# Kernel tuning notes

Measured on AMD Instinct MI355X. Metric: run time of the kernel, lower is better.

The kernel has to match this reference:

```python
import jax, jax.numpy as jnp
import numpy as np

N_NODES = 50000
N_EDGES = 800000
N_FEAT = 128
HIDDEN = 64
N_LAYERS = 3
N_GRAPHS = 512
N_CLASSES = 10
BN_EPS = 1e-5


def setup_inputs() -> dict:
    key = jax.random.key(0)
    ks = jax.random.split(key, 16)
    s = 1.0 / np.sqrt(HIDDEN)
    inp = {
        "x": jax.random.normal(ks[0], (N_NODES, N_FEAT), dtype=jnp.float32),
        "edge_index": jax.random.randint(ks[1], (2, N_EDGES), 0, N_NODES, dtype=jnp.int32),
        "batch": jnp.sort(jax.random.randint(ks[2], (N_NODES,), 0, N_GRAPHS, dtype=jnp.int32)),
        "enc_w": jax.random.normal(ks[3], (N_FEAT, HIDDEN), dtype=jnp.float32) / np.sqrt(N_FEAT),
        "enc_b": jnp.zeros((HIDDEN,), dtype=jnp.float32),
        "eps": jnp.zeros((N_LAYERS,), dtype=jnp.float32),
        "conv_w1": jax.random.normal(ks[4], (N_LAYERS, HIDDEN, HIDDEN), dtype=jnp.float32) * s,
        "conv_b1": jnp.zeros((N_LAYERS, HIDDEN), dtype=jnp.float32),
        "conv_w2": jax.random.normal(ks[5], (N_LAYERS, HIDDEN, HIDDEN), dtype=jnp.float32) * s,
        "conv_b2": jnp.zeros((N_LAYERS, HIDDEN), dtype=jnp.float32),
        "bn_gamma": jnp.ones((N_LAYERS, HIDDEN), dtype=jnp.float32),
        "bn_beta": jnp.zeros((N_LAYERS, HIDDEN), dtype=jnp.float32),
        "lin_w": jax.random.normal(ks[6], (HIDDEN, N_CLASSES), dtype=jnp.float32) * s,
        "lin_b": jnp.zeros((N_CLASSES,), dtype=jnp.float32),
    }
    return inp


def reference(x, edge_index, batch, enc_w, enc_b, eps, conv_w1, conv_b1,
              conv_w2, conv_b2, bn_gamma, bn_beta, lin_w, lin_b):
    n = x.shape[0]
    src, dst = edge_index[0], edge_index[1]
    h = x @ enc_w + enc_b  # [N, H] encoder
    for l in range(N_LAYERS):
        # GINConv: sum-aggregate neighbor features, add (1+eps)*self, 2-layer MLP
        agg = jax.ops.segment_sum(h[src], dst, num_segments=n)
        z = (1.0 + eps[l]) * h + agg
        z = jnp.maximum(z @ conv_w1[l] + conv_b1[l], 0.0) @ conv_w2[l] + conv_b2[l]
        # BatchNorm1d (batch statistics) + ReLU; dropout omitted (eval mode)
        mean = jnp.mean(z, axis=0)
        var = jnp.mean(jnp.square(z - mean), axis=0)
        z = (z - mean) * jax.lax.rsqrt(var + BN_EPS) * bn_gamma[l] + bn_beta[l]
        h = jnp.maximum(z, 0.0)
    # global mean pool over graphs
    pooled = jax.ops.segment_sum(h, batch, num_segments=N_GRAPHS)
    counts = jax.ops.segment_sum(jnp.ones((n,), dtype=h.dtype), batch, num_segments=N_GRAPHS)
    pooled = pooled / jnp.maximum(counts, 1.0)[:, None]
    return pooled @ lin_w + lin_b  # [N_GRAPHS, N_CLASSES]
```

## Files before the change

kernel.cpp:

```cpp
#include <hip/hip_runtime.h>

#define N_NODES   50000
#define N_EDGES   800000
#define N_FEAT    128
#define HIDDEN    64
#define N_LAYERS  3
#define N_GRAPHS  512
#define N_CLASSES 10
#define BN_EPS    1e-5f
#define SCAN_BLK  196
#define LWAVES    8
#define HP        32
#define NBLK      1024
#define QSCALE    65536.0f
#define QINV      (1.0f / 65536.0f)

__device__ __forceinline__ int swz(int c, int g) { return g ^ (c & 15); }

__device__ __forceinline__ unsigned bf16rne(float x)
{
    unsigned u = __float_as_uint(x);
    return (u + 0x7fffu + ((u >> 16) & 1u)) >> 16;
}
__device__ __forceinline__ float2 bf2(unsigned u)
{
    float2 r;
    r.x = __uint_as_float(u << 16);
    r.y = __uint_as_float(u & 0xffff0000u);
    return r;
}

__global__ __launch_bounds__(512, 6) void enc_kernel(
    const float* __restrict__ x, const float* __restrict__ w,
    const float* __restrict__ b, unsigned* __restrict__ h,
    int* __restrict__ deg)
{
    __shared__ __align__(16) float wT[HIDDEN * N_FEAT];
    __shared__ __align__(16) float xb[LWAVES][4][N_FEAT];
    {
        int g = blockIdx.x * 512 + threadIdx.x;
        if (g < N_NODES) deg[g] = 0;
    }
    for (int i = threadIdx.x; i < N_FEAT * HIDDEN; i += 512) {
        int k = i >> 6, c = i & 63;
        wT[c * 128 + swz(c, k >> 2) * 4 + (k & 3)] = w[i];
    }
    const int lane = threadIdx.x & 63;
    const int wv   = threadIdx.x >> 6;
    const int sz   = lane & 15;
    const int r2   = lane >> 5;
    const int cc   = (lane & 31) * 4;
    const float bias = b[lane];
    __syncthreads();
    const int nwaves = gridDim.x * LWAVES;
    for (int grp = blockIdx.x * LWAVES + wv; grp < N_NODES / 4; grp += nwaves) {
        const int nbase = grp * 4;
        float4 v0 = *(const float4*)&x[(size_t)(nbase + r2) * N_FEAT + cc];
        float4 v1 = *(const float4*)&x[(size_t)(nbase + 2 + r2) * N_FEAT + cc];
        *((float4*)&xb[wv][r2][cc])     = v0;
        *((float4*)&xb[wv][2 + r2][cc]) = v1;
        float o0 = bias, o1 = bias, o2 = bias, o3 = bias;
        #pragma unroll 8
        for (int kc = 0; kc < N_FEAT / 4; ++kc) {
            float4 w4 = *(const float4*)&wT[lane * 128 + ((kc ^ sz) << 2)];
            float4 z0 = *(const float4*)&xb[wv][0][4 * kc];
            float4 z1 = *(const float4*)&xb[wv][1][4 * kc];
            float4 z2 = *(const float4*)&xb[wv][2][4 * kc];
            float4 z3 = *(const float4*)&xb[wv][3][4 * kc];
            o0 = fmaf(w4.x, z0.x, fmaf(w4.y, z0.y, fmaf(w4.z, z0.z, fmaf(w4.w, z0.w, o0))));
            o1 = fmaf(w4.x, z1.x, fmaf(w4.y, z1.y, fmaf(w4.z, z1.z, fmaf(w4.w, z1.w, o1))));
            o2 = fmaf(w4.x, z2.x, fmaf(w4.y, z2.y, fmaf(w4.z, z2.z, fmaf(w4.w, z2.w, o2))));
            o3 = fmaf(w4.x, z3.x, fmaf(w4.y, z3.y, fmaf(w4.z, z3.z, fmaf(w4.w, z3.w, o3))));
        }
        float t0 = __shfl_xor(o0, 1), t1 = __shfl_xor(o1, 1);
        float t2 = __shfl_xor(o2, 1), t3 = __shfl_xor(o3, 1);
        if (!(lane & 1)) {
            int p = lane >> 1;
            h[(size_t)(nbase + 0) * HP + p] = bf16rne(o0) | (bf16rne(t0) << 16);
            h[(size_t)(nbase + 1) * HP + p] = bf16rne(o1) | (bf16rne(t1) << 16);
            h[(size_t)(nbase + 2) * HP + p] = bf16rne(o2) | (bf16rne(t2) << 16);
            h[(size_t)(nbase + 3) * HP + p] = bf16rne(o3) | (bf16rne(t3) << 16);
        }
    }
}

__global__ __launch_bounds__(256) void hist_kernel(const int* __restrict__ ei,
                                                   int* __restrict__ deg)
{
    int e = blockIdx.x * 256 + threadIdx.x;
    if (e < N_EDGES) atomicAdd(&deg[ei[N_EDGES + e]], 1);
}

__global__ __launch_bounds__(256) void scan1_kernel(const int* __restrict__ deg,
                                                    int* __restrict__ row_start,
                                                    int* __restrict__ bsum)
{
    __shared__ int s[256];
    const int tid = threadIdx.x;
    const int gid = blockIdx.x * 256 + tid;
    int v = (gid < N_NODES) ? deg[gid] : 0;
    s[tid] = v;
    __syncthreads();
    for (int off = 1; off < 256; off <<= 1) {
        int t = (tid >= off) ? s[tid - off] : 0;
        __syncthreads();
        if (tid >= off) s[tid] += t;
        __syncthreads();
    }
    if (gid < N_NODES) row_start[gid] = s[tid] - v;
    if (tid == 255) bsum[blockIdx.x] = s[255];
}

__global__ __launch_bounds__(256) void scan2_kernel(int* __restrict__ bsum,
                                                    int* __restrict__ row_start)
{
    __shared__ int s[256];
    const int tid = threadIdx.x;
    int v = (tid < SCAN_BLK) ? bsum[tid] : 0;
    s[tid] = v;
    __syncthreads();
    for (int off = 1; off < 256; off <<= 1) {
        int t = (tid >= off) ? s[tid - off] : 0;
        __syncthreads();
        if (tid >= off) s[tid] += t;
        __syncthreads();
    }
    if (tid < SCAN_BLK) bsum[tid] = s[tid] - v;
    if (tid == 255) row_start[N_NODES] = s[255];
}

__global__ __launch_bounds__(256) void scan3_kernel(int* __restrict__ row_start,
                                                    const int* __restrict__ bsum,
                                                    int* __restrict__ cursor)
{
    int gid = blockIdx.x * 256 + threadIdx.x;
    if (gid < N_NODES) {
        int v = row_start[gid] + bsum[blockIdx.x];
        row_start[gid] = v;
        cursor[gid] = v;
    }
}

__global__ __launch_bounds__(256) void fill_kernel(const int* __restrict__ ei,
                                                   int* __restrict__ cursor,
                                                   int* __restrict__ csr_src)
{
    int e = blockIdx.x * 256 + threadIdx.x;
    if (e >= N_EDGES) return;
    int d = ei[N_EDGES + e];
    int pos = atomicAdd(&cursor[d], 1);
    csr_src[pos] = ei[e];
}

template<bool HASBN>
__global__ __launch_bounds__(512, 8) void layer_kernel(
    const unsigned* __restrict__ hin, const int* __restrict__ csr_src,
    const int* __restrict__ row_start,
    const float* __restrict__ stats_prev, const float* __restrict__ gamma,
    const float* __restrict__ beta,
    const float* __restrict__ eps, int layer,
    const float* __restrict__ w1, const float* __restrict__ b1,
    const float* __restrict__ w2, const float* __restrict__ b2,
    unsigned* __restrict__ hout, float* __restrict__ partials)
{
    __shared__ __align__(16) float wT1[HIDDEN * HIDDEN];
    __shared__ __align__(16) float wT2[HIDDEN * HIDDEN];
    __shared__ __align__(16) float zb[LWAVES][4][HIDDEN];
    for (int i = threadIdx.x; i < HIDDEN * HIDDEN; i += 512) {
        int k = i >> 6, c = i & 63;
        int dst = c * 64 + swz(c, k >> 2) * 4 + (k & 3);
        wT1[dst] = w1[i];
        wT2[dst] = w2[i];
    }
    const int lane = threadIdx.x & 63;
    const int wv   = threadIdx.x >> 6;
    const int o    = lane >> 3;
    const int c8   = (lane & 7) * 4;
    const int cb   = c8 * 2;
    const int sz   = lane & 15;
    float Ag[8], Bg[8];
    #pragma unroll
    for (int t = 0; t < 8; ++t) { Ag[t] = 1.f; Bg[t] = 0.f; }
    if (HASBN) {
        const float invN = 1.0f / (float)N_NODES;
        #pragma unroll
        for (int t = 0; t < 8; ++t) {
            float mean = stats_prev[cb + t] * invN;
            float var  = stats_prev[HIDDEN + cb + t] * invN - mean * mean;
            float inv  = rsqrtf(fmaxf(var, 0.f) + BN_EPS);
            Ag[t] = inv * gamma[cb + t];
            Bg[t] = beta[cb + t] - mean * Ag[t];
        }
    }
    const float sf  = 1.0f + eps[layer];
    const float b1c = b1[lane], b2c = b2[lane];
    __syncthreads();

    float s = 0.f, s2 = 0.f;
    const int nwaves = gridDim.x * LWAVES;
    for (int grp = blockIdx.x * LWAVES + wv; grp < N_NODES / 4; grp += nwaves) {
        const int nbase = grp * 4;
        #pragma unroll
        for (int n = 0; n < 4; ++n) {
            const int node = nbase + n;
            const int s0 = row_start[node];
            const int s1 = row_start[node + 1];
            int a[8];
            #pragma unroll
            for (int t = 0; t < 8; ++t) a[t] = 0;
            for (int jb = s0; jb < s1; jb += 64) {
                int m = s1 - jb; if (m > 64) m = 64;
                int idx = csr_src[jb + (lane < m ? lane : m - 1)];
                int mm = m & ~7;
                for (int j = 0; j < mm; j += 8) {
                    int i = __shfl(idx, j + o);
                    uint4 u = *(const uint4*)&hin[(size_t)i * HP + c8];
                    float2 f0 = bf2(u.x), f1 = bf2(u.y), f2 = bf2(u.z), f3 = bf2(u.w);
                    float v[8] = {f0.x, f0.y, f1.x, f1.y, f2.x, f2.y, f3.x, f3.y};
                    #pragma unroll
                    for (int t = 0; t < 8; ++t) {
                        float f = v[t];
                        if (HASBN) f = fmaxf(fmaf(f, Ag[t], Bg[t]), 0.f);
                        a[t] += (int)(f * QSCALE);
                    }
                }
                int r8 = m & 7;
                if (r8) {
                    int sl = mm + o;
                    int i = __shfl(idx, sl < m ? sl : m - 1);
                    if (o < r8) {
                        uint4 u = *(const uint4*)&hin[(size_t)i * HP + c8];
                        float2 f0 = bf2(u.x), f1 = bf2(u.y), f2 = bf2(u.z), f3 = bf2(u.w);
                        float v[8] = {f0.x, f0.y, f1.x, f1.y, f2.x, f2.y, f3.x, f3.y};
                        #pragma unroll
                        for (int t = 0; t < 8; ++t) {
                            float f = v[t];
                            if (HASBN) f = fmaxf(fmaf(f, Ag[t], Bg[t]), 0.f);
                            a[t] += (int)(f * QSCALE);
                        }
                    }
                }
            }
            #pragma unroll
            for (int t = 0; t < 8; ++t) {
                a[t] += __shfl_xor(a[t], 8);
                a[t] += __shfl_xor(a[t], 16);
                a[t] += __shfl_xor(a[t], 32);
            }
            if (o == 0) {
                uint4 su = *(const uint4*)&hin[(size_t)node * HP + c8];
                float2 g0 = bf2(su.x), g1 = bf2(su.y), g2 = bf2(su.z), g3 = bf2(su.w);
                float svv[8] = {g0.x, g0.y, g1.x, g1.y, g2.x, g2.y, g3.x, g3.y};
                float zo[8];
                #pragma unroll
                for (int t = 0; t < 8; ++t) {
                    float f = svv[t];
                    if (HASBN) f = fmaxf(fmaf(f, Ag[t], Bg[t]), 0.f);
                    zo[t] = fmaf(sf, f, (float)a[t] * QINV);
                }
                float4 q0 = {zo[0], zo[1], zo[2], zo[3]};
                float4 q1 = {zo[4], zo[5], zo[6], zo[7]};
                *((float4*)&zb[wv][n][cb])     = q0;
                *((float4*)&zb[wv][n][cb + 4]) = q1;
            }
        }
        float o0 = b1c, o1 = b1c, o2 = b1c, o3 = b1c;
        #pragma unroll 4
        for (int kc = 0; kc < HIDDEN / 4; ++kc) {
            float4 w4 = *(const float4*)&wT1[lane * 64 + ((kc ^ sz) << 2)];
            float4 z0 = *(const float4*)&zb[wv][0][4 * kc];
            float4 z1 = *(const float4*)&zb[wv][1][4 * kc];
            float4 z2 = *(const float4*)&zb[wv][2][4 * kc];
            float4 z3 = *(const float4*)&zb[wv][3][4 * kc];
            o0 = fmaf(w4.x, z0.x, fmaf(w4.y, z0.y, fmaf(w4.z, z0.z, fmaf(w4.w, z0.w, o0))));
            o1 = fmaf(w4.x, z1.x, fmaf(w4.y, z1.y, fmaf(w4.z, z1.z, fmaf(w4.w, z1.w, o1))));
            o2 = fmaf(w4.x, z2.x, fmaf(w4.y, z2.y, fmaf(w4.z, z2.z, fmaf(w4.w, z2.w, o2))));
            o3 = fmaf(w4.x, z3.x, fmaf(w4.y, z3.y, fmaf(w4.z, z3.z, fmaf(w4.w, z3.w, o3))));
        }
        zb[wv][0][lane] = fmaxf(o0, 0.f);
        zb[wv][1][lane] = fmaxf(o1, 0.f);
        zb[wv][2][lane] = fmaxf(o2, 0.f);
        zb[wv][3][lane] = fmaxf(o3, 0.f);
        float p0 = b2c, p1 = b2c, p2 = b2c, p3 = b2c;
        #pragma unroll 4
        for (int kc = 0; kc < HIDDEN / 4; ++kc) {
            float4 w4 = *(const float4*)&wT2[lane * 64 + ((kc ^ sz) << 2)];
            float4 z0 = *(const float4*)&zb[wv][0][4 * kc];
            float4 z1 = *(const float4*)&zb[wv][1][4 * kc];
            float4 z2 = *(const float4*)&zb[wv][2][4 * kc];
            float4 z3 = *(const float4*)&zb[wv][3][4 * kc];
            p0 = fmaf(w4.x, z0.x, fmaf(w4.y, z0.y, fmaf(w4.z, z0.z, fmaf(w4.w, z0.w, p0))));
            p1 = fmaf(w4.x, z1.x, fmaf(w4.y, z1.y, fmaf(w4.z, z1.z, fmaf(w4.w, z1.w, p1))));
            p2 = fmaf(w4.x, z2.x, fmaf(w4.y, z2.y, fmaf(w4.z, z2.z, fmaf(w4.w, z2.w, p2))));
            p3 = fmaf(w4.x, z3.x, fmaf(w4.y, z3.y, fmaf(w4.z, z3.z, fmaf(w4.w, z3.w, p3))));
        }
        float t0 = __shfl_xor(p0, 1), t1 = __shfl_xor(p1, 1);
        float t2 = __shfl_xor(p2, 1), t3 = __shfl_xor(p3, 1);
        if (!(lane & 1)) {
            int p = lane >> 1;
            hout[(size_t)(nbase + 0) * HP + p] = bf16rne(p0) | (bf16rne(t0) << 16);
            hout[(size_t)(nbase + 1) * HP + p] = bf16rne(p1) | (bf16rne(t1) << 16);
            hout[(size_t)(nbase + 2) * HP + p] = bf16rne(p2) | (bf16rne(t2) << 16);
            hout[(size_t)(nbase + 3) * HP + p] = bf16rne(p3) | (bf16rne(t3) << 16);
        }
        s  += ((p0 + p1) + (p2 + p3));
        s2 += ((p0 * p0 + p1 * p1) + (p2 * p2 + p3 * p3));
    }
    __syncthreads();
    float* red = &zb[0][0][0];
    red[threadIdx.x] = s;
    red[512 + threadIdx.x] = s2;
    __syncthreads();
    if (wv == 0) {
        float ts = 0.f, ts2 = 0.f;
        #pragma unroll
        for (int wq = 0; wq < LWAVES; ++wq) {
            ts  += red[wq * 64 + lane];
            ts2 += red[512 + wq * 64 + lane];
        }
        partials[(size_t)blockIdx.x * 128 + lane]      = ts;
        partials[(size_t)blockIdx.x * 128 + 64 + lane] = ts2;
    }
}

__global__ __launch_bounds__(1024) void stats_reduce_kernel(
    const float* __restrict__ partials, float* __restrict__ stats)
{
    __shared__ float red[8][128];
    const int c = threadIdx.x & 127;
    const int k = threadIdx.x >> 7;
    float s = 0.f;
    #pragma unroll 4
    for (int b = k * 128; b < (k + 1) * 128; ++b)
        s += partials[(size_t)b * 128 + c];
    red[k][c] = s;
    __syncthreads();
    if (k == 0) {
        float t = 0.f;
        #pragma unroll
        for (int kk = 0; kk < 8; ++kk) t += red[kk][c];
        stats[c] = t;
    }
}

__device__ __forceinline__ int lbound(const int* __restrict__ a, int n, int v)
{
    int lo = 0, hi = n;
    while (lo < hi) { int m = (lo + hi) >> 1; if (a[m] < v) lo = m + 1; else hi = m; }
    return lo;
}

__global__ __launch_bounds__(256) void pool_kernel(
    const unsigned* __restrict__ hpre, const int* __restrict__ batch,
    const float* __restrict__ stats, const float* __restrict__ gamma,
    const float* __restrict__ beta, float* __restrict__ pooled)
{
    __shared__ int bounds[2];
    __shared__ float red[256];
    const int g = blockIdx.x;
    if (threadIdx.x < 2)
        bounds[threadIdx.x] = lbound(batch, N_NODES, g + threadIdx.x);
    __syncthreads();
    const int start = bounds[0], end = bounds[1];
    const int col = threadIdx.x & 63;
    const int row = threadIdx.x >> 6;
    const float invN = 1.0f / (float)N_NODES;
    float mean = stats[col] * invN;
    float var  = stats[HIDDEN + col] * invN - mean * mean;
    float inv  = rsqrtf(fmaxf(var, 0.f) + BN_EPS);
    float A = inv * gamma[col];
    float B = beta[col] - mean * A;
    float s = 0.f;
    for (int r = start + row; r < end; r += 4) {
        unsigned u = hpre[(size_t)r * HP + (col >> 1)];
        float v = (col & 1) ? __uint_as_float(u & 0xffff0000u)
                            : __uint_as_float(u << 16);
        s += fmaxf(fmaf(v, A, B), 0.f);
    }
    red[threadIdx.x] = s;
    __syncthreads();
    if (row == 0) {
        float t = red[col] + red[64 + col] + red[128 + col] + red[192 + col];
        pooled[(size_t)g * HIDDEN + col] = t / fmaxf((float)(end - start), 1.0f);
    }
}

__global__ void out_kernel(const float* __restrict__ pooled,
                           const float* __restrict__ w, const float* __restrict__ b,
                           float* __restrict__ out)
{
    int gid = blockIdx.x * blockDim.x + threadIdx.x;
    if (gid >= N_GRAPHS * N_CLASSES) return;
    int g = gid / N_CLASSES;
    int c = gid - g * N_CLASSES;
    float acc = b[c];
    for (int j = 0; j < HIDDEN; ++j)
        acc = fmaf(pooled[(size_t)g * HIDDEN + j], w[j * N_CLASSES + c], acc);
    out[gid] = acc;
}

extern "C" void kernel_launch(void* const* d_in, const int* in_sizes, int n_in,
                              void* d_out, int out_size, void* d_ws, size_t ws_size,
                              hipStream_t stream)
{
    const float* x       = (const float*)d_in[0];
    const int*   ei      = (const int*)d_in[1];
    const int*   batch   = (const int*)d_in[2];
    const float* enc_w   = (const float*)d_in[3];
    const float* enc_b   = (const float*)d_in[4];
    const float* eps     = (const float*)d_in[5];
    const float* conv_w1 = (const float*)d_in[6];
    const float* conv_b1 = (const float*)d_in[7];
    const float* conv_w2 = (const float*)d_in[8];
    const float* conv_b2 = (const float*)d_in[9];
    const float* bn_g    = (const float*)d_in[10];
    const float* bn_b    = (const float*)d_in[11];
    const float* lin_w   = (const float*)d_in[12];
    const float* lin_b   = (const float*)d_in[13];
    float* out = (float*)d_out;

    char* ws = (char*)d_ws;
    const size_t HB = (size_t)N_NODES * HP * sizeof(unsigned);
    size_t off = 0;
    unsigned* P    = (unsigned*)(ws + off); off += HB;
    unsigned* Q    = (unsigned*)(ws + off); off += HB;
    float* stats   = (float*)(ws + off); off += N_LAYERS * 2 * HIDDEN * sizeof(float);
    float* pooled  = (float*)(ws + off); off += (size_t)N_GRAPHS * HIDDEN * sizeof(float);
    float* partials= (float*)(ws + off); off += (size_t)NBLK * 128 * sizeof(float);
    int* deg       = (int*)(ws + off); off += 50176 * sizeof(int);
    int* row_start = (int*)(ws + off); off += 50176 * sizeof(int);
    int* cursor    = (int*)(ws + off); off += 50176 * sizeof(int);
    int* bsum      = (int*)(ws + off); off += 256 * sizeof(int);
    int* csr_src   = (int*)(ws + off); off += (size_t)N_EDGES * sizeof(int);

    enc_kernel<<<768, 512, 0, stream>>>(x, enc_w, enc_b, P, deg);

    hist_kernel<<<(N_EDGES + 255) / 256, 256, 0, stream>>>(ei, deg);
    scan1_kernel<<<SCAN_BLK, 256, 0, stream>>>(deg, row_start, bsum);
    scan2_kernel<<<1, 256, 0, stream>>>(bsum, row_start);
    scan3_kernel<<<SCAN_BLK, 256, 0, stream>>>(row_start, bsum, cursor);
    fill_kernel<<<(N_EDGES + 255) / 256, 256, 0, stream>>>(ei, cursor, csr_src);

    const unsigned* curin = P;
    unsigned* curout = Q;
    for (int l = 0; l < N_LAYERS; ++l) {
        const float* w1 = conv_w1 + (size_t)l * HIDDEN * HIDDEN;
        const float* b1 = conv_b1 + (size_t)l * HIDDEN;
        const float* w2 = conv_w2 + (size_t)l * HIDDEN * HIDDEN;
        const float* b2 = conv_b2 + (size_t)l * HIDDEN;
        if (l == 0)
            layer_kernel<false><<<NBLK, 512, 0, stream>>>(
                curin, csr_src, row_start, nullptr, nullptr, nullptr,
                eps, l, w1, b1, w2, b2, curout, partials);
        else
            layer_kernel<true><<<NBLK, 512, 0, stream>>>(
                curin, csr_src, row_start,
                stats + (size_t)(l - 1) * 2 * HIDDEN,
                bn_g + (size_t)(l - 1) * HIDDEN, bn_b + (size_t)(l - 1) * HIDDEN,
                eps, l, w1, b1, w2, b2, curout, partials);
        stats_reduce_kernel<<<1, 1024, 0, stream>>>(partials,
                                                    stats + (size_t)l * 2 * HIDDEN);
        const unsigned* t = curout; curout = (unsigned*)curin; curin = t;
    }

    pool_kernel<<<N_GRAPHS, 256, 0, stream>>>(
        Q, batch, stats + (size_t)(N_LAYERS - 1) * 2 * HIDDEN,
        bn_g + (size_t)(N_LAYERS - 1) * HIDDEN, bn_b + (size_t)(N_LAYERS - 1) * HIDDEN,
        pooled);
    out_kernel<<<(N_GRAPHS * N_CLASSES + 255) / 256, 256, 0, stream>>>(pooled, lin_w, lin_b, out);
}
```

Before: 332.6 us.

## Move BN apply to separate pass, atomic work queue, fixed-point atomic stats

Pulls the BatchNorm+ReLU application out of the per-edge gather loop into a separate bn_apply pass over h, so neighbour gathers no longer do an FMA and max per element. Replaces the per-block partials plus a single-block stats reduction with 64-bit fixed-point atomics. Switches node-group scheduling to a dynamic atomic work counter for load balance. Fuses the pooling and output linear kernels. The extra bn_apply pass adds a full read-modify-write of h per layer, and the fixed-point statistics could lose precision or overflow.

After: 906.5 us. +172.5%, slower.

```diff
diff --git a/kernel.cpp b/kernel.cpp
--- a/kernel.cpp
+++ b/kernel.cpp
@@ -12,8 +12,11 @@
 #define LWAVES    8
 #define HP        32
 #define NBLK      1024
+#define NGRP      (N_NODES / 4)
 #define QSCALE    65536.0f
 #define QINV      (1.0f / 65536.0f)
+#define SSCALE    1048576.0
+#define SINV      (1.0 / 1048576.0)
 
 __device__ __forceinline__ int swz(int c, int g) { return g ^ (c & 15); }
 
@@ -28,6 +31,19 @@
     r.x = __uint_as_float(u << 16);
     r.y = __uint_as_float(u & 0xffff0000u);
     return r;
+}
+
+__device__ __forceinline__ void bn_const(const unsigned long long* stats,
+                                         const float* gamma, const float* beta,
+                                         int c, float& A, float& B)
+{
+    double m  = (double)(long long)stats[c]          * (SINV / (double)N_NODES);
+    double e2 = (double)(long long)stats[HIDDEN + c] * (SINV / (double)N_NODES);
+    float mean = (float)m;
+    float var  = (float)(e2 - m * m);
+    float inv  = rsqrtf(fmaxf(var, 0.f) + BN_EPS);
+    A = inv * gamma[c];
+    B = beta[c] - mean * A;
 }
 
 __global__ __launch_bounds__(512, 6) void enc_kernel(
@@ -53,7 +69,7 @@
     const float bias = b[lane];
     __syncthreads();
     const int nwaves = gridDim.x * LWAVES;
-    for (int grp = blockIdx.x * LWAVES + wv; grp < N_NODES / 4; grp += nwaves) {
+    for (int grp = blockIdx.x * LWAVES + wv; grp < NGRP; grp += nwaves) {
         const int nbase = grp * 4;
         float4 v0 = *(const float4*)&x[(size_t)(nbase + r2) * N_FEAT + cc];
         float4 v1 = *(const float4*)&x[(size_t)(nbase + 2 + r2) * N_FEAT + cc];
@@ -85,8 +101,14 @@
 }
 
 __global__ __launch_bounds__(256) void hist_kernel(const int* __restrict__ ei,
-                                                   int* __restrict__ deg)
-{
+                                                   int* __restrict__ deg,
+                                                   unsigned long long* __restrict__ stats,
+                                                   int* __restrict__ wctr)
+{
+    if (blockIdx.x == 0) {
+        for (int i = threadIdx.x; i < N_LAYERS * 2 * HIDDEN; i += 256) stats[i] = 0ull;
+        if (threadIdx.x < N_LAYERS) wctr[threadIdx.x] = 0;
+    }
     int e = blockIdx.x * 256 + threadIdx.x;
     if (e < N_EDGES) atomicAdd(&deg[ei[N_EDGES + e]], 1);
 }
@@ -152,16 +174,13 @@
     csr_src[pos] = ei[e];
 }
 
-template<bool HASBN>
 __global__ __launch_bounds__(512, 8) void layer_kernel(
     const unsigned* __restrict__ hin, const int* __restrict__ csr_src,
-    const int* __restrict__ row_start,
-    const float* __restrict__ stats_prev, const float* __restrict__ gamma,
-    const float* __restrict__ beta,
+    const int* __restrict__ row_start, int* __restrict__ wctr,
     const float* __restrict__ eps, int layer,
     const float* __restrict__ w1, const float* __restrict__ b1,
     const float* __restrict__ w2, const float* __restrict__ b2,
-    unsigned* __restrict__ hout, float* __restrict__ partials)
+    unsigned* __restrict__ hout, unsigned long long* __restrict__ stats_cur)
 {
     __shared__ __align__(16) float wT1[HIDDEN * HIDDEN];
     __shared__ __align__(16) float wT2[HIDDEN * HIDDEN];
@@ -178,27 +197,16 @@
     const int c8   = (lane & 7) * 4;
     const int cb   = c8 * 2;
     const int sz   = lane & 15;
-    float Ag[8], Bg[8];
-    #pragma unroll
-    for (int t = 0; t < 8; ++t) { Ag[t] = 1.f; Bg[t] = 0.f; }
-    if (HASBN) {
-        const float invN = 1.0f / (float)N_NODES;
-        #pragma unroll
-        for (int t = 0; t < 8; ++t) {
-            float mean = stats_prev[cb + t] * invN;
-            float var  = stats_prev[HIDDEN + cb + t] * invN - mean * mean;
-            float inv  = rsqrtf(fmaxf(var, 0.f) + BN_EPS);
-            Ag[t] = inv * gamma[cb + t];
-            Bg[t] = beta[cb + t] - mean * Ag[t];
-        }
-    }
     const float sf  = 1.0f + eps[layer];
     const float b1c = b1[lane], b2c = b2[lane];
     __syncthreads();
 
-    float s = 0.f, s2 = 0.f;
-    const int nwaves = gridDim.x * LWAVES;
-    for (int grp = blockIdx.x * LWAVES + wv; grp < N_NODES / 4; grp += nwaves) {
+    long long sAcc = 0, s2Acc = 0;
+    for (;;) {
+        int grp = 0;
+        if (lane == 0) grp = atomicAdd(wctr, 1);
+        grp = __shfl(grp, 0);
+        if (grp >= NGRP) break;
         const int nbase = grp * 4;
         #pragma unroll
         for (int n = 0; n < 4; ++n) {
@@ -216,13 +224,10 @@
                     int i = __shfl(idx, j + o);
                     uint4 u = *(const uint4*)&hin[(size_t)i * HP + c8];
                     float2 f0 = bf2(u.x), f1 = bf2(u.y), f2 = bf2(u.z), f3 = bf2(u.w);
-                    float v[8] = {f0.x, f0.y, f1.x, f1.y, f2.x, f2.y, f3.x, f3.y};
-                    #pragma unroll
-                    for (int t = 0; t < 8; ++t) {
-                        float f = v[t];
-                        if (HASBN) f = fmaxf(fmaf(f, Ag[t], Bg[t]), 0.f);
-                        a[t] += (int)(f * QSCALE);
-                    }
+                    a[0] += (int)(f0.x * QSCALE); a[1] += (int)(f0.y * QSCALE);
+                    a[2] += (int)(f1.x * QSCALE); a[3] += (int)(f1.y * QSCALE);
+                    a[4] += (int)(f2.x * QSCALE); a[5] += (int)(f2.y * QSCALE);
+                    a[6] += (int)(f3.x * QSCALE); a[7] += (int)(f3.y * QSCALE);
                 }
                 int r8 = m & 7;
                 if (r8) {
@@ -231,13 +236,10 @@
                     if (o < r8) {
                         uint4 u = *(const uint4*)&hin[(size_t)i * HP + c8];
                         float2 f0 = bf2(u.x), f1 = bf2(u.y), f2 = bf2(u.z), f3 = bf2(u.w);
-                        float v[8] = {f0.x, f0.y, f1.x, f1.y, f2.x, f2.y, f3.x, f3.y};
-                        #pragma unroll
-                        for (int t = 0; t < 8; ++t) {
-                            float f = v[t];
-                            if (HASBN) f = fmaxf(fmaf(f, Ag[t], Bg[t]), 0.f);
-                            a[t] += (int)(f * QSCALE);
-                        }
+                        a[0] += (int)(f0.x * QSCALE); a[1] += (int)(f0.y * QSCALE);
+                        a[2] += (int)(f1.x * QSCALE); a[3] += (int)(f1.y * QSCALE);
+                        a[4] += (int)(f2.x * QSCALE); a[5] += (int)(f2.y * QSCALE);
+                        a[6] += (int)(f3.x * QSCALE); a[7] += (int)(f3.y * QSCALE);
                     }
                 }
             }
@@ -253,11 +255,8 @@
                 float svv[8] = {g0.x, g0.y, g1.x, g1.y, g2.x, g2.y, g3.x, g3.y};
                 float zo[8];
                 #pragma unroll
-                for (int t = 0; t < 8; ++t) {
-                    float f = svv[t];
-                    if (HASBN) f = fmaxf(fmaf(f, Ag[t], Bg[t]), 0.f);
-                    zo[t] = fmaf(sf, f, (float)a[t] * QINV);
-                }
+                for (int t = 0; t < 8; ++t)
+                    zo[t] = fmaf(sf, svv[t], (float)a[t] * QINV);
                 float4 q0 = {zo[0], zo[1], zo[2], zo[3]};
                 float4 q1 = {zo[4], zo[5], zo[6], zo[7]};
                 *((float4*)&zb[wv][n][cb])     = q0;
@@ -303,44 +302,50 @@
             hout[(size_t)(nbase + 2) * HP + p] = bf16rne(p2) | (bf16rne(t2) << 16);
             hout[(size_t)(nbase + 3) * HP + p] = bf16rne(p3) | (bf16rne(t3) << 16);
         }
-        s  += ((p0 + p1) + (p2 + p3));
-        s2 += ((p0 * p0 + p1 * p1) + (p2 * p2 + p3 * p3));
-    }
-    __syncthreads();
-    float* red = &zb[0][0][0];
-    red[threadIdx.x] = s;
-    red[512 + threadIdx.x] = s2;
+        float g1 = (p0 + p1) + (p2 + p3);
+        float g2 = (p0 * p0 + p1 * p1) + (p2 * p2 + p3 * p3);
+        sAcc  += (long long)((double)g1 * SSCALE);
+        s2Acc += (long long)((double)g2 * SSCALE);
+    }
+    __syncthreads();
+    long long* red = (long long*)&zb[0][0][0];
+    red[threadIdx.x]       = sAcc;
+    red[512 + threadIdx.x] = s2Acc;
     __syncthreads();
     if (wv == 0) {
-        float ts = 0.f, ts2 = 0.f;
+        long long ts = 0, ts2 = 0;
         #pragma unroll
         for (int wq = 0; wq < LWAVES; ++wq) {
             ts  += red[wq * 64 + lane];
             ts2 += red[512 + wq * 64 + lane];
         }
-        partials[(size_t)blockIdx.x * 128 + lane]      = ts;
-        partials[(size_t)blockIdx.x * 128 + 64 + lane] = ts2;
-    }
-}
-
-__global__ __launch_bounds__(1024) void stats_reduce_kernel(
-    const float* __restrict__ partials, float* __restrict__ stats)
-{
-    __shared__ float red[8][128];
-    const int c = threadIdx.x & 127;
-    const int k = threadIdx.x >> 7;
-    float s = 0.f;
-    #pragma unroll 4
-    for (int b = k * 128; b < (k + 1) * 128; ++b)
-        s += partials[(size_t)b * 128 + c];
-    red[k][c] = s;
-    __syncthreads();
-    if (k == 0) {
-        float t = 0.f;
-        #pragma unroll
-        for (int kk = 0; kk < 8; ++kk) t += red[kk][c];
-        stats[c] = t;
-    }
+        atomicAdd((unsigned long long*)&stats_cur[lane],          (unsigned long long)ts);
+        atomicAdd((unsigned long long*)&stats_cur[HIDDEN + lane], (unsigned long long)ts2);
+    }
+}
+
+__global__ __launch_bounds__(512) void bn_apply_kernel(
+    unsigned* __restrict__ h, const unsigned long long* __restrict__ stats,
+    const float* __restrict__ gamma, const float* __restrict__ beta)
+{
+    int gid = blockIdx.x * 512 + threadIdx.x;
+    if (gid >= N_NODES * 8) return;
+    const int cb = (gid & 7) * 8;
+    float A[8], B[8];
+    #pragma unroll
+    for (int t = 0; t < 8; ++t) bn_const(stats, gamma, beta, cb + t, A[t], B[t]);
+    uint4 u = *((const uint4*)h + gid);
+    float2 f0 = bf2(u.x), f1 = bf2(u.y), f2 = bf2(u.z), f3 = bf2(u.w);
+    float v[8] = {f0.x, f0.y, f1.x, f1.y, f2.x, f2.y, f3.x, f3.y};
+    unsigned w[4];
+    #pragma unroll
+    for (int t = 0; t < 4; ++t) {
+        float lo = fmaxf(fmaf(v[2 * t],     A[2 * t],     B[2 * t]),     0.f);
+        float hi = fmaxf(fmaf(v[2 * t + 1], A[2 * t + 1], B[2 * t + 1]), 0.f);
+        w[t] = bf16rne(lo) | (bf16rne(hi) << 16);
+    }
+    uint4 ov = {w[0], w[1], w[2], w[3]};
+    *((uint4*)h + gid) = ov;
 }
 
 __device__ __forceinline__ int lbound(const int* __restrict__ a, int n, int v)
@@ -350,13 +355,15 @@
     return lo;
 }
 
-__global__ __launch_bounds__(256) void pool_kernel(
+__global__ __launch_bounds__(256) void pool_out_kernel(
     const unsigned* __restrict__ hpre, const int* __restrict__ batch,
-    const float* __restrict__ stats, const float* __restrict__ gamma,
-    const float* __restrict__ beta, float* __restrict__ pooled)
+    const unsigned long long* __restrict__ stats, const float* __restrict__ gamma,
+    const float* __restrict__ beta, const float* __restrict__ lw,
+    const float* __restrict__ lb, float* __restrict__ out)
 {
     __shared__ int bounds[2];
     __shared__ float red[256];
+    __shared__ float pv[64];
     const int g = blockIdx.x;
     if (threadIdx.x < 2)
         bounds[threadIdx.x] = lbound(batch, N_NODES, g + threadIdx.x);
@@ -364,12 +371,8 @@
     const int start = bounds[0], end = bounds[1];
     const int col = threadIdx.x & 63;
     const int row = threadIdx.x >> 6;
-    const float invN = 1.0f / (float)N_NODES;
-    float mean = stats[col] * invN;
-    float var  = stats[HIDDEN + col] * invN - mean * mean;
-    float inv  = rsqrtf(fmaxf(var, 0.f) + BN_EPS);
-    float A = inv * gamma[col];
-    float B = beta[col] - mean * A;
+    float A, B;
+    bn_const(stats, gamma, beta, col, A, B);
     float s = 0.f;
     for (int r = start + row; r < end; r += 4) {
         unsigned u = hpre[(size_t)r * HP + (col >> 1)];
@@ -381,22 +384,16 @@
     __syncthreads();
     if (row == 0) {
         float t = red[col] + red[64 + col] + red[128 + col] + red[192 + col];
-        pooled[(size_t)g * HIDDEN + col] = t / fmaxf((float)(end - start), 1.0f);
-    }
-}
-
-__global__ void out_kernel(const float* __restrict__ pooled,
-                           const float* __restrict__ w, const float* __restrict__ b,
-                           float* __restrict__ out)
-{
-    int gid = blockIdx.x * blockDim.x + threadIdx.x;
-    if (gid >= N_GRAPHS * N_CLASSES) return;
-    int g = gid / N_CLASSES;
-    int c = gid - g * N_CLASSES;
-    float acc = b[c];
-    for (int j = 0; j < HIDDEN; ++j)
-        acc = fmaf(pooled[(size_t)g * HIDDEN + j], w[j * N_CLASSES + c], acc);
-    out[gid] = acc;
+        pv[col] = t / fmaxf((float)(end - start), 1.0f);
+    }
+    __syncthreads();
+    if (threadIdx.x < N_CLASSES) {
+        float acc = lb[threadIdx.x];
+        #pragma unroll 16
+        for (int j = 0; j < HIDDEN; ++j)
+            acc = fmaf(pv[j], lw[j * N_CLASSES + threadIdx.x], acc);
+        out[g * N_CLASSES + threadIdx.x] = acc;
+    }
 }
 
 extern "C" void kernel_launch(void* const* d_in, const int* in_sizes, int n_in,
@@ -424,9 +421,9 @@
     size_t off = 0;
     unsigned* P    = (unsigned*)(ws + off); off += HB;
     unsigned* Q    = (unsigned*)(ws + off); off += HB;
-    float* stats   = (float*)(ws + off); off += N_LAYERS * 2 * HIDDEN * sizeof(float);
-    float* pooled  = (float*)(ws + off); off += (size_t)N_GRAPHS * HIDDEN * sizeof(float);
-    float* partials= (float*)(ws + off); off += (size_t)NBLK * 128 * sizeof(float);
+    unsigned long long* stats64 = (unsigned long long*)(ws + off);
+    off += N_LAYERS * 2 * HIDDEN * sizeof(unsigned long long);
+    int* wctr      = (int*)(ws + off); off += 16 * sizeof(int);
     int* deg       = (int*)(ws + off); off += 50176 * sizeof(int);
     int* row_start = (int*)(ws + off); off += 50176 * sizeof(int);
     int* cursor    = (int*)(ws + off); off += 50176 * sizeof(int);
@@ -435,12 +432,13 @@
 
     enc_kernel<<<768, 512, 0, stream>>>(x, enc_w, enc_b, P, deg);
 
-    hist_kernel<<<(N_EDGES + 255) / 256, 256, 0, stream>>>(ei, deg);
+    hist_kernel<<<(N_EDGES + 255) / 256, 256, 0, stream>>>(ei, deg, stats64, wctr);
     scan1_kernel<<<SCAN_BLK, 256, 0, stream>>>(deg, row_start, bsum);
     scan2_kernel<<<1, 256, 0, stream>>>(bsum, row_start);
     scan3_kernel<<<SCAN_BLK, 256, 0, stream>>>(row_start, bsum, cursor);
     fill_kernel<<<(N_EDGES + 255) / 256, 256, 0, stream>>>(ei, cursor, csr_src);
 
+    const int bn_grid = (N_NODES * 8 + 511) / 512;
     const unsigned* curin = P;
     unsigned* curout = Q;
     for (int l = 0; l < N_LAYERS; ++l) {
@@ -448,24 +446,18 @@
         const float* b1 = conv_b1 + (size_t)l * HIDDEN;
         const float* w2 = conv_w2 + (size_t)l * HIDDEN * HIDDEN;
         const float* b2 = conv_b2 + (size_t)l * HIDDEN;
-        if (l == 0)
-            layer_kernel<false><<<NBLK, 512, 0, stream>>>(
-                curin, csr_src, row_start, nullptr, nullptr, nullptr,
-                eps, l, w1, b1, w2, b2, curout, partials);
-        else
-            layer_kernel<true><<<NBLK, 512, 0, stream>>>(
-                curin, csr_src, row_start,
-                stats + (size_t)(l - 1) * 2 * HIDDEN,
-                bn_g + (size_t)(l - 1) * HIDDEN, bn_b + (size_t)(l - 1) * HIDDEN,
-                eps, l, w1, b1, w2, b2, curout, partials);
-        stats_reduce_kernel<<<1, 1024, 0, stream>>>(partials,
-                                                    stats + (size_t)l * 2 * HIDDEN);
+        layer_kernel<<<NBLK, 512, 0, stream>>>(
+            curin, csr_src, row_start, wctr + l, eps, l,
+            w1, b1, w2, b2, curout, stats64 + (size_t)l * 2 * HIDDEN);
+        if (l < N_LAYERS - 1)
+            bn_apply_kernel<<<bn_grid, 512, 0, stream>>>(
+                curout, stats64 + (size_t)l * 2 * HIDDEN,
+                bn_g + (size_t)l * HIDDEN, bn_b + (size_t)l * HIDDEN);
         const unsigned* t = curout; curout = (unsigned*)curin; curin = t;
     }
 
-    pool_kernel<<<N_GRAPHS, 256, 0, stream>>>(
-        Q, batch, stats + (size_t)(N_LAYERS - 1) * 2 * HIDDEN,
+    pool_out_kernel<<<N_GRAPHS, 256, 0, stream>>>(
+        Q, batch, stats64 + (size_t)(N_LAYERS - 1) * 2 * HIDDEN,
         bn_g + (size_t)(N_LAYERS - 1) * HIDDEN, bn_b + (size_t)(N_LAYERS - 1) * HIDDEN,
-        pooled);
-    out_kernel<<<(N_GRAPHS * N_CLASSES + 255) / 256, 256, 0, stream>>>(pooled, lin_w, lin_b, out);
-}
+        lin_w, lin_b, out);
+}
```
